# Kernel tuning notes

Hardware: AMD Instinct MI355X
Metric: run time of the kernel (lower is better)

Reference implementation:

```python
import jax, jax.numpy as jnp
import numpy as np

V, BLOCK, L, H, C = 50257, 1024, 4, 12, 768
HS = C // H  # 64
EPS = 1e-6  # flax LayerNorm default


def _ln(x, scale, bias):
    mu = jnp.mean(x, axis=-1, keepdims=True)
    var = jnp.var(x, axis=-1, keepdims=True)
    return (x - mu) * jax.lax.rsqrt(var + EPS) * scale + bias


def setup_inputs() -> dict:
    key = jax.random.key(0)
    ks = jax.random.split(key, 12)
    B, T = 2, 1024
    inp = {
        'idx': jax.random.randint(ks[0], (B, T), 0, V),
        'targets': jax.random.randint(ks[1], (B, T), 0, V),
        'wte': jax.random.normal(ks[2], (V, C), jnp.float32) * 0.02,
        'wpe': jax.random.normal(ks[3], (BLOCK, C), jnp.float32) * 0.02,
        'ln1_s': jnp.ones((L, C), jnp.float32),
        'ln1_b': jnp.zeros((L, C), jnp.float32),
        'attn_k': jax.random.normal(ks[4], (L, C, H, 3 * HS), jnp.float32) * 0.02,
        'attn_b': jnp.zeros((L, H, 3 * HS), jnp.float32),
        'aproj_k': jax.random.normal(ks[5], (L, C, C), jnp.float32) * 0.02,
        'aproj_b': jnp.zeros((L, C), jnp.float32),
        'ln2_s': jnp.ones((L, C), jnp.float32),
        'ln2_b': jnp.zeros((L, C), jnp.float32),
        'fc_k': jax.random.normal(ks[6], (L, C, 4 * C), jnp.float32) * 0.02,
        'fc_b': jnp.zeros((L, 4 * C), jnp.float32),
        'mproj_k': jax.random.normal(ks[7], (L, 4 * C, C), jnp.float32) * 0.02,
        'mproj_b': jnp.zeros((L, C), jnp.float32),
        'lnf_s': jnp.ones((C,), jnp.float32),
        'lnf_b': jnp.zeros((C,), jnp.float32),
    }
    return inp


def _block(x, ln1_s, ln1_b, Wqkv, bqkv, Wo, bo, ln2_s, ln2_b, Wfc, bfc, Wmp, bmp, mask):
    B, T, _ = x.shape
    h = _ln(x, ln1_s, ln1_b)
    qkv = jnp.einsum('btc,chd->bhtd', h, Wqkv) + bqkv[:, None, :]  # [B,H,T,3HS]
    q, k, v = jnp.split(qkv, 3, axis=-1)
    att = jnp.einsum('bhtd,bhsd->bhts', q, k) * (1.0 / jnp.sqrt(jnp.float32(HS)))
    att = jnp.where(mask, att, -jnp.inf)
    att = jax.nn.softmax(att, axis=-1)
    y = jnp.einsum('bhts,bhsd->bthd', att, v).reshape(B, T, C)
    x = x + y @ Wo + bo
    h = _ln(x, ln2_s, ln2_b)
    h = jax.nn.gelu(h @ Wfc + bfc, approximate=True)
    x = x + h @ Wmp + bmp
    return x


def reference(idx, targets, wte, wpe, ln1_s, ln1_b, attn_k, attn_b, aproj_k, aproj_b,
              ln2_s, ln2_b, fc_k, fc_b, mproj_k, mproj_b, lnf_s, lnf_b):
    B, T = idx.shape
    x = wte[idx] + wpe[jnp.arange(T)][None]  # [B,T,C]
    mask = jnp.tril(jnp.ones((T, T), bool))[None, None]
    for l in range(L):
        x = _block(x, ln1_s[l], ln1_b[l], attn_k[l], attn_b[l], aproj_k[l], aproj_b[l],
                   ln2_s[l], ln2_b[l], fc_k[l], fc_b[l], mproj_k[l], mproj_b[l], mask)
    x = _ln(x, lnf_s, lnf_b)
    logits = jnp.einsum('btc,vc->btv', x, wte)  # tied output projection (wte.attend)
    logp = jax.nn.log_softmax(logits, axis=-1)
    loss = -jnp.mean(jnp.take_along_axis(logp, targets[..., None], axis=-1))
    return logits, loss
```

## Files before the change

### kernel.cpp

```cpp
#include <hip/hip_runtime.h>
#include <hip/hip_bf16.h>
#include <math.h>

typedef __attribute__((ext_vector_type(8))) short bf16x8;
typedef __attribute__((ext_vector_type(4))) float f32x4;

static constexpr int Bv   = 2;
static constexpr int Tv   = 1024;
static constexpr int Cv   = 768;
static constexpr int Hv   = 12;
static constexpr int Lv   = 4;
static constexpr int Vv   = 50257;
static constexpr int Mv   = 2048;
static constexpr int NTv  = 393;
static constexpr float EPSv = 1e-6f;

__device__ __forceinline__ void gload16(const void* g, void* l) {
    __builtin_amdgcn_global_load_lds((const __attribute__((address_space(1))) void*)g,
                                     (__attribute__((address_space(3))) void*)l, 16, 0, 0);
}
__device__ __forceinline__ void waitvm0_barrier() {
    asm volatile("s_waitcnt vmcnt(0)" ::: "memory");
    __builtin_amdgcn_s_barrier();
}

__global__ void embed_kernel(const int* __restrict__ idx,
                             const float* __restrict__ wte,
                             const float* __restrict__ wpe,
                             float* __restrict__ x) {
    int row = blockIdx.x;
    int t   = row & (Tv - 1);
    int tok = idx[row];
    const float* src = wte + (size_t)tok * Cv;
    const float* pos = wpe + (size_t)t * Cv;
    float* dst = x + (size_t)row * Cv;
    for (int c = threadIdx.x; c < Cv; c += 256)
        dst[c] = src[c] + pos[c];
}

__device__ __forceinline__ ushort4 pack4bf(float4 v) {
    ushort4 u;
    u.x = __bfloat16_as_ushort(__float2bfloat16(v.x));
    u.y = __bfloat16_as_ushort(__float2bfloat16(v.y));
    u.z = __bfloat16_as_ushort(__float2bfloat16(v.z));
    u.w = __bfloat16_as_ushort(__float2bfloat16(v.w));
    return u;
}

__global__ void ln_kernel(const float* __restrict__ in,
                          const float* __restrict__ sc,
                          const float* __restrict__ bi,
                          __hip_bfloat16* __restrict__ out) {
    int row  = blockIdx.x * 4 + (threadIdx.x >> 6);
    int lane = threadIdx.x & 63;
    const float4* xr = (const float4*)(in + (size_t)row * Cv);
    float4 a = xr[lane], b = xr[lane + 64], c = xr[lane + 128];
    float sum = a.x + a.y + a.z + a.w + b.x + b.y + b.z + b.w + c.x + c.y + c.z + c.w;
    float sq  = a.x*a.x + a.y*a.y + a.z*a.z + a.w*a.w
              + b.x*b.x + b.y*b.y + b.z*b.z + b.w*b.w
              + c.x*c.x + c.y*c.y + c.z*c.z + c.w*c.w;
    #pragma unroll
    for (int off = 32; off; off >>= 1) {
        sum += __shfl_xor(sum, off, 64);
        sq  += __shfl_xor(sq,  off, 64);
    }
    float mean = sum * (1.0f / Cv);
    float var  = sq * (1.0f / Cv) - mean * mean;
    float rs   = rsqrtf(var + EPSv);
    const float4* s4 = (const float4*)sc;
    const float4* b4 = (const float4*)bi;
    ushort4* orow = (ushort4*)(out + (size_t)row * Cv);
    #pragma unroll
    for (int i = 0; i < 3; ++i) {
        float4 v = (i == 0) ? a : (i == 1) ? b : c;
        float4 s = s4[lane + 64 * i];
        float4 t = b4[lane + 64 * i];
        float4 o;
        o.x = (v.x - mean) * rs * s.x + t.x;
        o.y = (v.y - mean) * rs * s.y + t.y;
        o.z = (v.z - mean) * rs * s.z + t.z;
        o.w = (v.w - mean) * rs * s.w + t.w;
        orow[lane + 64 * i] = pack4bf(o);
    }
}

__global__ void wtrans_kernel(const float* __restrict__ in,
                              __hip_bfloat16* __restrict__ out, int K, int N) {
    __shared__ float tile[32][33];
    int k0 = blockIdx.y * 32, n0 = blockIdx.x * 32;
    int tx = threadIdx.x & 31, ty = threadIdx.x >> 5;
    #pragma unroll
    for (int i = 0; i < 4; ++i)
        tile[ty + i * 8][tx] = in[(size_t)(k0 + ty + i * 8) * N + n0 + tx];
    __syncthreads();
    #pragma unroll
    for (int i = 0; i < 4; ++i)
        out[(size_t)(n0 + ty + i * 8) * K + k0 + tx] =
            __float2bfloat16(tile[tx][ty + i * 8]);
}

__global__ void cvt_kernel(const float* __restrict__ in,
                           __hip_bfloat16* __restrict__ out, int n4) {
    int stride = gridDim.x * 256;
    for (int i = blockIdx.x * 256 + threadIdx.x; i < n4; i += stride) {
        float4 v = ((const float4*)in)[i];
        ((ushort4*)out)[i] = pack4bf(v);
    }
}

__global__ void vtrans_kernel(const __hip_bfloat16* __restrict__ qkv,
                              __hip_bfloat16* __restrict__ vt) {
    __shared__ __hip_bfloat16 tile[32][33];
    int bh = blockIdx.z;
    int b = bh / Hv, h = bh % Hv;
    int t0 = blockIdx.x * 32, d0 = blockIdx.y * 32;
    int tx = threadIdx.x & 31, ty = threadIdx.x >> 5;
    #pragma unroll
    for (int i = 0; i < 4; ++i)
        tile[ty + i * 8][tx] =
            qkv[(size_t)(b * Tv + t0 + ty + i * 8) * 2304 + h * 192 + 128 + d0 + tx];
    __syncthreads();
    #pragma unroll
    for (int i = 0; i < 4; ++i)
        vt[((size_t)bh * 64 + d0 + ty + i * 8) * Tv + t0 + tx] = tile[tx][ty + i * 8];
}

template<int EPI, int BM>
__launch_bounds__(256)
__global__ void gemm_bf16(const __hip_bfloat16* __restrict__ A,
                          const __hip_bfloat16* __restrict__ Bt,
                          const float* __restrict__ bias,
                          const float* R, float* Cf,
                          __hip_bfloat16* __restrict__ Cb,
                          int M, int N, int K) {
    constexpr int FM = BM / 32;
    constexpr int NA = BM / 64;
    __shared__ __hip_bfloat16 As[2][BM * 32];
    __shared__ __hip_bfloat16 Bs[2][64 * 32];
    int tid = threadIdx.x;
    int wave = tid >> 6, lane = tid & 63;
    int wr = wave >> 1, wc = wave & 1;
    int rowBase = blockIdx.y * BM, colBase = blockIdx.x * 64;

    f32x4 acc[FM][2] = {};

    int srow  = wave * 16 + (lane >> 2);
    int skcol = (lane & 3) * 8;
    const __hip_bfloat16* Ap0 = A + (size_t)(rowBase + srow) * K + skcol;
    const __hip_bfloat16* Ap1 = (NA > 1) ? (Ap0 + (size_t)64 * K) : Ap0;
    const __hip_bfloat16* Bp0 = Bt + (size_t)(colBase + srow) * K + skcol;
    int ldso = wave * 512;

    int aoff = (wr * (BM / 2) + (lane & 15)) * 32 + (lane >> 4) * 8;
    int boff = (wc * 32 + (lane & 15)) * 32 + (lane >> 4) * 8;

    gload16(Ap0, &As[0][ldso]);
    if constexpr (NA > 1) gload16(Ap1, &As[0][2048 + ldso]);
    gload16(Bp0, &Bs[0][ldso]);
    Ap0 += 32; Ap1 += 32; Bp0 += 32;
    waitvm0_barrier();

    int nt = K / 32;
    for (int t = 0; t < nt - 1; ++t) {
        int cur = t & 1, nxt = cur ^ 1;
        gload16(Ap0, &As[nxt][ldso]);
        if constexpr (NA > 1) gload16(Ap1, &As[nxt][2048 + ldso]);
        gload16(Bp0, &Bs[nxt][ldso]);
        Ap0 += 32; Ap1 += 32; Bp0 += 32;

        bf16x8 av[FM], bv[2];
        #pragma unroll
        for (int m = 0; m < FM; ++m) av[m] = *(const bf16x8*)&As[cur][aoff + m * 512];
        #pragma unroll
        for (int n = 0; n < 2; ++n)  bv[n] = *(const bf16x8*)&Bs[cur][boff + n * 512];
        #pragma unroll
        for (int m = 0; m < FM; ++m)
            #pragma unroll
            for (int n = 0; n < 2; ++n)
                acc[m][n] = __builtin_amdgcn_mfma_f32_16x16x32_bf16(
                    av[m], bv[n], acc[m][n], 0, 0, 0);
        waitvm0_barrier();
    }
    {
        int cur = (nt - 1) & 1;
        bf16x8 av[FM], bv[2];
        #pragma unroll
        for (int m = 0; m < FM; ++m) av[m] = *(const bf16x8*)&As[cur][aoff + m * 512];
        #pragma unroll
        for (int n = 0; n < 2; ++n)  bv[n] = *(const bf16x8*)&Bs[cur][boff + n * 512];
        #pragma unroll
        for (int m = 0; m < FM; ++m)
            #pragma unroll
            for (int n = 0; n < 2; ++n)
                acc[m][n] = __builtin_amdgcn_mfma_f32_16x16x32_bf16(
                    av[m], bv[n], acc[m][n], 0, 0, 0);
    }

    int fq = lane >> 4, fr = lane & 15;
    #pragma unroll
    for (int m = 0; m < FM; ++m) {
        #pragma unroll
        for (int n = 0; n < 2; ++n) {
            f32x4 v = acc[m][n];
            int col = colBase + wc * 32 + n * 16 + fr;
            #pragma unroll
            for (int j = 0; j < 4; ++j) {
                int row = rowBase + wr * (BM / 2) + m * 16 + fq * 4 + j;
                float val = v[j] + bias[col];
                if (EPI == 1) {
                    val += R[(size_t)row * N + col];
                    Cf[(size_t)row * N + col] = val;
                } else {
                    if (EPI == 2) {
                        float u = val;
                        float cc = 0.7978845608028654f * (u + 0.044715f * u * u * u);
                        val = 0.5f * u * (1.0f + tanhf(cc));
                    }
                    Cb[(size_t)row * N + col] = __float2bfloat16(val);
                }
            }
        }
    }
}

__launch_bounds__(256)
__global__ void attn_kernel(const __hip_bfloat16* __restrict__ qkv,
                            const __hip_bfloat16* __restrict__ vt,
                            __hip_bfloat16* __restrict__ att) {
    __shared__ __hip_bfloat16 Qs[64 * 64];
    __shared__ __hip_bfloat16 Ks[64 * 64];
    __shared__ __hip_bfloat16 Vs[64 * 64];
    __shared__ __hip_bfloat16 Ps[64 * 64];
    int bh = blockIdx.x;
    int b = bh / Hv, h = bh % Hv;
    int qt = (int)gridDim.y - 1 - (int)blockIdx.y;
    int q0 = qt * 64;
    int tid = threadIdx.x, wave = tid >> 6, lane = tid & 63;
    int g = lane >> 4, fr = lane & 15;
    int srow8 = lane >> 3, sc8 = lane & 7;

    const __hip_bfloat16* qbase = qkv + (size_t)(b * Tv + q0) * 2304 + h * 192;
    #pragma unroll
    for (int i = 0; i < 2; ++i) {
        int row = wave * 16 + i * 8 + srow8;
        gload16(qbase + (size_t)row * 2304 + ((sc8 ^ (row & 7)) * 8),
                Qs + (wave * 16 + i * 8) * 64);
    }

    f32x4 accO[4] = {};
    float mrun[4] = {-1e30f, -1e30f, -1e30f, -1e30f};
    float lrun[4] = {0.f, 0.f, 0.f, 0.f};

    for (int kv = 0; kv <= qt; ++kv) {
        int s0 = kv * 64;
        __syncthreads();
        const __hip_bfloat16* kbase = qkv + (size_t)(b * Tv + s0) * 2304 + h * 192 + 64;
        const __hip_bfloat16* vbase = vt + (size_t)bh * 64 * Tv + s0;
        #pragma unroll
        for (int i = 0; i < 2; ++i) {
            int row = wave * 16 + i * 8 + srow8;
            gload16(kbase + (size_t)row * 2304 + ((sc8 ^ (row & 7)) * 8),
                    Ks + (wave * 16 + i * 8) * 64);
            gload16(vbase + (size_t)row * Tv + ((sc8 ^ (row & 7)) * 8),
                    Vs + (wave * 16 + i * 8) * 64);
        }
        __syncthreads();

        f32x4 s4[4] = {};
        #pragma unroll
        for (int kk = 0; kk < 2; ++kk) {
            int qrow = wave * 16 + fr;
            bf16x8 qa = *(const bf16x8*)&Qs[qrow * 64 + (((g + 4 * kk) ^ (fr & 7)) * 8)];
            #pragma unroll
            for (int n = 0; n < 4; ++n) {
                int krow = n * 16 + fr;
                bf16x8 kb = *(const bf16x8*)&Ks[krow * 64 + (((g + 4 * kk) ^ (fr & 7)) * 8)];
                s4[n] = __builtin_amdgcn_mfma_f32_16x16x32_bf16(qa, kb, s4[n], 0, 0, 0);
            }
        }

        bool dia = (kv == qt);
        #pragma unroll
        for (int j = 0; j < 4; ++j) {
            int qg = q0 + wave * 16 + g * 4 + j;
            float sj[4], mx = -1e30f;
            #pragma unroll
            for (int n = 0; n < 4; ++n) {
                float v = s4[n][j] * 0.125f;
                if (dia && (s0 + n * 16 + fr) > qg) v = -1e30f;
                sj[n] = v;
                mx = fmaxf(mx, v);
            }
            #pragma unroll
            for (int off = 1; off < 16; off <<= 1)
                mx = fmaxf(mx, __shfl_xor(mx, off, 64));
            float mnew = fmaxf(mrun[j], mx);
            float ps = 0.f;
            unsigned short pb[4];
            #pragma unroll
            for (int n = 0; n < 4; ++n) {
                float p = __expf(sj[n] - mnew);
                __hip_bfloat16 pc = __float2bfloat16(p);
                pb[n] = __bfloat16_as_ushort(pc);
                ps += __bfloat162float(pc);
            }
            #pragma unroll
            for (int off = 1; off < 16; off <<= 1)
                ps += __shfl_xor(ps, off, 64);
            float cr = __expf(mrun[j] - mnew);
            lrun[j] = lrun[j] * cr + ps;
            mrun[j] = mnew;
            int prow = wave * 16 + g * 4 + j;
            #pragma unroll
            for (int n = 0; n < 4; ++n) {
                int byteoff = (32 * n + 2 * fr) ^ ((prow & 7) << 4);
                ((unsigned short*)Ps)[prow * 64 + (byteoff >> 1)] = pb[n];
            }
            #pragma unroll
            for (int n = 0; n < 4; ++n) accO[n][j] *= cr;
        }
        __syncthreads();

        #pragma unroll
        for (int kk = 0; kk < 2; ++kk) {
            int prow = wave * 16 + fr;
            bf16x8 pa = *(const bf16x8*)&Ps[prow * 64 + (((g + 4 * kk) ^ (fr & 7)) * 8)];
            #pragma unroll
            for (int n = 0; n < 4; ++n) {
                int vrow = n * 16 + fr;
                bf16x8 vb = *(const bf16x8*)&Vs[vrow * 64 + (((g + 4 * kk) ^ (fr & 7)) * 8)];
                accO[n] = __builtin_amdgcn_mfma_f32_16x16x32_bf16(pa, vb, accO[n], 0, 0, 0);
            }
        }
    }

    #pragma unroll
    for (int j = 0; j < 4; ++j) {
        float inv = 1.0f / lrun[j];
        int row = b * Tv + q0 + wave * 16 + g * 4 + j;
        #pragma unroll
        for (int n = 0; n < 4; ++n)
            att[(size_t)row * Cv + h * 64 + n * 16 + fr] =
                __float2bfloat16(accO[n][j] * inv);
    }
}

__launch_bounds__(256)
__global__ void lmhead_kernel(const __hip_bfloat16* __restrict__ A,
                              const __hip_bfloat16* __restrict__ Bt,
                              float* __restrict__ Cf,
                              float* __restrict__ pLse) {
    constexpr int K = Cv, N = Vv;
    __shared__ __hip_bfloat16 As[2][4096];
    __shared__ __hip_bfloat16 Bs[2][4096];
    __shared__ float ps2[2][128];

    int bid = blockIdx.x;
    int nid = (bid & 7) * (NTv * 16 / 8) + (bid >> 3);
    int rowT = nid & 15, colT = nid >> 4;
    int rowBase = rowT * 128, colBase = colT * 128;

    int tid = threadIdx.x, wave = tid >> 6, lane = tid & 63;
    int wr = wave >> 1, wc = wave & 1;

    f32x4 acc[4][4] = {};

    int srow  = wave * 16 + (lane >> 2);
    int skcol = (lane & 3) * 8;
    const __hip_bfloat16* Ap  = A + (size_t)(rowBase + srow) * K + skcol;
    const __hip_bfloat16* Ap2 = Ap + (size_t)64 * K;
    int brow1 = colBase + srow;
    int brow2 = brow1 + 64;
    const __hip_bfloat16* Bp  = Bt + (size_t)brow1 * K + skcol;
    const __hip_bfloat16* Bp2 = Bt + (size_t)(brow2 < N ? brow2 : N - 1) * K + skcol;
    int ldso = wave * 512;

    int aoff = (wr * 64 + (lane & 15)) * 32 + (lane >> 4) * 8;
    int boff = (wc * 64 + (lane & 15)) * 32 + (lane >> 4) * 8;

    gload16(Ap,  &As[0][ldso]);
    gload16(Ap2, &As[0][2048 + ldso]);
    gload16(Bp,  &Bs[0][ldso]);
    gload16(Bp2, &Bs[0][2048 + ldso]);
    Ap += 32; Ap2 += 32; Bp += 32; Bp2 += 32;
    waitvm0_barrier();

    constexpr int nt = K / 32;
    for (int t = 0; t < nt - 1; ++t) {
        int cur = t & 1, nxt = cur ^ 1;
        gload16(Ap,  &As[nxt][ldso]);
        gload16(Ap2, &As[nxt][2048 + ldso]);
        gload16(Bp,  &Bs[nxt][ldso]);
        gload16(Bp2, &Bs[nxt][2048 + ldso]);
        Ap += 32; Ap2 += 32; Bp += 32; Bp2 += 32;

        bf16x8 av[4], bv[4];
        #pragma unroll
        for (int m = 0; m < 4; ++m) av[m] = *(const bf16x8*)&As[cur][aoff + m * 512];
        #pragma unroll
        for (int n = 0; n < 4; ++n) bv[n] = *(const bf16x8*)&Bs[cur][boff + n * 512];
        #pragma unroll
        for (int m = 0; m < 4; ++m)
            #pragma unroll
            for (int n = 0; n < 4; ++n)
                acc[m][n] = __builtin_amdgcn_mfma_f32_16x16x32_bf16(
                    av[m], bv[n], acc[m][n], 0, 0, 0);
        waitvm0_barrier();
    }
    {
        int cur = (nt - 1) & 1;
        bf16x8 av[4], bv[4];
        #pragma unroll
        for (int m = 0; m < 4; ++m) av[m] = *(const bf16x8*)&As[cur][aoff + m * 512];
        #pragma unroll
        for (int n = 0; n < 4; ++n) bv[n] = *(const bf16x8*)&Bs[cur][boff + n * 512];
        #pragma unroll
        for (int m = 0; m < 4; ++m)
            #pragma unroll
            for (int n = 0; n < 4; ++n)
                acc[m][n] = __builtin_amdgcn_mfma_f32_16x16x32_bf16(
                    av[m], bv[n], acc[m][n], 0, 0, 0);
    }

    int fq = lane >> 4, fr = lane & 15;

    #pragma unroll
    for (int m = 0; m < 4; ++m) {
        #pragma unroll
        for (int j = 0; j < 4; ++j) {
            int row = rowBase + wr * 64 + m * 16 + fq * 4 + j;
            float s = 0.f;
            #pragma unroll
            for (int n = 0; n < 4; ++n) {
                int col = colBase + wc * 64 + n * 16 + fr;
                float v = acc[m][n][j];
                if (col < N) {
                    Cf[(size_t)row * N + col] = v;
                    s += __expf(v);
                }
            }
            #pragma unroll
            for (int off = 1; off < 16; off <<= 1)
                s += __shfl_xor(s, off, 64);
            if (fr == 0)
                ps2[wc][wr * 64 + m * 16 + fq * 4 + j] = s;
        }
    }
    __syncthreads();
    if (tid < 128)
        pLse[(size_t)(rowBase + tid) * NTv + colT] = ps2[0][tid] + ps2[1][tid];
}

__global__ void plse_reduce_kernel(const float* __restrict__ pLse,
                                   const float* __restrict__ logits,
                                   const int* __restrict__ targets,
                                   float* __restrict__ rloss) {
    int row  = blockIdx.x * 4 + (threadIdx.x >> 6);
    int lane = threadIdx.x & 63;
    const float* pr = pLse + (size_t)row * NTv;
    float l = 0.f;
    for (int i = lane; i < NTv; i += 64) l += pr[i];
    #pragma unroll
    for (int off = 32; off; off >>= 1) l += __shfl_xor(l, off, 64);
    if (lane == 0)
        rloss[row] = logf(l) - logits[(size_t)row * Vv + targets[row]];
}

__global__ void loss_final_kernel(const float* __restrict__ rloss,
                                  float* __restrict__ out, int out_size) {
    float s = 0.f;
    for (int i = threadIdx.x; i < Mv; i += 256) s += rloss[i];
    #pragma unroll
    for (int off = 32; off; off >>= 1) s += __shfl_xor(s, off, 64);
    __shared__ float sw[4];
    int wave = threadIdx.x >> 6, lane = threadIdx.x & 63;
    if (lane == 0) sw[wave] = s;
    __syncthreads();
    if (threadIdx.x == 0)
        out[out_size - 1] = (sw[0] + sw[1] + sw[2] + sw[3]) / (float)Mv;
}

extern "C" void kernel_launch(void* const* d_in, const int* in_sizes, int n_in,
                              void* d_out, int out_size, void* d_ws, size_t ws_size,
                              hipStream_t stream) {
    const int*   idx     = (const int*)  d_in[0];
    const int*   targets = (const int*)  d_in[1];
    const float* wte     = (const float*)d_in[2];
    const float* wpe     = (const float*)d_in[3];
    const float* ln1_s   = (const float*)d_in[4];
    const float* ln1_b   = (const float*)d_in[5];
    const float* attn_k  = (const float*)d_in[6];
    const float* attn_b  = (const float*)d_in[7];
    const float* aproj_k = (const float*)d_in[8];
    const float* aproj_b = (const float*)d_in[9];
    const float* ln2_s   = (const float*)d_in[10];
    const float* ln2_b   = (const float*)d_in[11];
    const float* fc_k    = (const float*)d_in[12];
    const float* fc_b    = (const float*)d_in[13];
    const float* mproj_k = (const float*)d_in[14];
    const float* mproj_b = (const float*)d_in[15];
    const float* lnf_s   = (const float*)d_in[16];
    const float* lnf_b   = (const float*)d_in[17];

    float* out = (float*)d_out;
    char* ws  = (char*)d_ws;
    char* ob  = (char*)d_out;

    constexpr size_t NEED = 83568128ULL;
    if (ws_size < NEED) return;

    __hip_bfloat16* wte_bf = (__hip_bfloat16*)(ws + 0);
    __hip_bfloat16* h_bf   = (__hip_bfloat16*)(ws + 77194752);
    float*          pLse   = (float*)(ws + 80340480);
    float*          rloss  = (float*)(ws + 83559936);

    float*          x      = (float*)(ob + 0);
    __hip_bfloat16* qkv_bf = (__hip_bfloat16*)(ob + 6291456);
    __hip_bfloat16* vt_bf  = (__hip_bfloat16*)(ob + 15728640);
    __hip_bfloat16* att_bf = (__hip_bfloat16*)(ob + 18874368);
    __hip_bfloat16* fco_bf = (__hip_bfloat16*)(ob + 22020096);
    __hip_bfloat16* w0     = (__hip_bfloat16*)(ob + 34603008);
    __hip_bfloat16* w1     = (__hip_bfloat16*)(ob + 38141952);
    __hip_bfloat16* w2     = (__hip_bfloat16*)(ob + 39321600);
    __hip_bfloat16* w3     = (__hip_bfloat16*)(ob + 44040192);

    embed_kernel<<<Mv, 256, 0, stream>>>(idx, wte, wpe, x);

    for (int l = 0; l < Lv; ++l) {
        wtrans_kernel<<<dim3(72, 24), 256, 0, stream>>>(
            attn_k + (size_t)l * Cv * 2304, w0, Cv, 2304);
        wtrans_kernel<<<dim3(24, 24), 256, 0, stream>>>(
            aproj_k + (size_t)l * Cv * Cv, w1, Cv, Cv);
        wtrans_kernel<<<dim3(96, 24), 256, 0, stream>>>(
            fc_k + (size_t)l * Cv * 3072, w2, Cv, 3072);
        wtrans_kernel<<<dim3(24, 96), 256, 0, stream>>>(
            mproj_k + (size_t)l * 3072 * Cv, w3, 3072, Cv);

        ln_kernel<<<512, 256, 0, stream>>>(x, ln1_s + l * Cv, ln1_b + l * Cv, h_bf);
        gemm_bf16<0, 128><<<dim3(36, 16), 256, 0, stream>>>(
            h_bf, w0, attn_b + l * 2304, nullptr, nullptr, qkv_bf, Mv, 2304, Cv);
        vtrans_kernel<<<dim3(32, 2, 24), 256, 0, stream>>>(qkv_bf, vt_bf);
        attn_kernel<<<dim3(24, 16), 256, 0, stream>>>(qkv_bf, vt_bf, att_bf);
        gemm_bf16<1, 64><<<dim3(12, 32), 256, 0, stream>>>(
            att_bf, w1, aproj_b + l * Cv, x, x, nullptr, Mv, Cv, Cv);
        ln_kernel<<<512, 256, 0, stream>>>(x, ln2_s + l * Cv, ln2_b + l * Cv, h_bf);
        gemm_bf16<2, 128><<<dim3(48, 16), 256, 0, stream>>>(
            h_bf, w2, fc_b + l * 3072, nullptr, nullptr, fco_bf, Mv, 3072, Cv);
        gemm_bf16<1, 64><<<dim3(12, 32), 256, 0, stream>>>(
            fco_bf, w3, mproj_b + l * Cv, x, x, nullptr, Mv, Cv, 3072);
    }

    ln_kernel<<<512, 256, 0, stream>>>(x, lnf_s, lnf_b, h_bf);
    cvt_kernel<<<2048, 256, 0, stream>>>(wte, wte_bf, (Vv * Cv) / 4);
    lmhead_kernel<<<16 * NTv, 256, 0, stream>>>(h_bf, wte_bf, out, pLse);
    plse_reduce_kernel<<<512, 256, 0, stream>>>(pLse, out, targets, rloss);
    loss_final_kernel<<<1, 256, 0, stream>>>(rloss, out, out_size);
}
```

Before: 1.063 ms.

## Triple-buffer LDS tiles with partial vmcnt waits in GEMM and LM head

Both the generic bf16 GEMM and the LM-head GEMM move from double buffering to three LDS stages, keeping two tiles of global-to-LDS loads in flight. Partial s_waitcnt vmcnt counts replace full drains, and an lgkmcnt barrier after the fragment reads lets the next stage overwrite the buffer just consumed. The aim is to hide global load latency behind MFMA work. The cost is 50% more LDS per block, which may lower occupancy, especially in the LM head at 48KB.

```diff
diff --git a/kernel.cpp b/kernel.cpp
--- a/kernel.cpp
+++ b/kernel.cpp
@@ -19,9 +19,17 @@
     __builtin_amdgcn_global_load_lds((const __attribute__((address_space(1))) void*)g,
                                      (__attribute__((address_space(3))) void*)l, 16, 0, 0);
 }
-__device__ __forceinline__ void waitvm0_barrier() {
-    asm volatile("s_waitcnt vmcnt(0)" ::: "memory");
-    __builtin_amdgcn_s_barrier();
+template<int N>
+__device__ __forceinline__ void waitvm_barrier() {
+    if constexpr (N == 0)      asm volatile("s_waitcnt vmcnt(0)\ns_barrier" ::: "memory");
+    else if constexpr (N == 2) asm volatile("s_waitcnt vmcnt(2)\ns_barrier" ::: "memory");
+    else if constexpr (N == 3) asm volatile("s_waitcnt vmcnt(3)\ns_barrier" ::: "memory");
+    else if constexpr (N == 4) asm volatile("s_waitcnt vmcnt(4)\ns_barrier" ::: "memory");
+    else if constexpr (N == 6) asm volatile("s_waitcnt vmcnt(6)\ns_barrier" ::: "memory");
+    else                       asm volatile("s_waitcnt vmcnt(8)\ns_barrier" ::: "memory");
+}
+__device__ __forceinline__ void lgkm0_barrier() {
+    asm volatile("s_waitcnt lgkmcnt(0)\ns_barrier" ::: "memory");
 }
 
 __global__ void embed_kernel(const int* __restrict__ idx,
@@ -133,10 +141,11 @@
                           const float* R, float* Cf,
                           __hip_bfloat16* __restrict__ Cb,
                           int M, int N, int K) {
-    constexpr int FM = BM / 32;
-    constexpr int NA = BM / 64;
-    __shared__ __hip_bfloat16 As[2][BM * 32];
-    __shared__ __hip_bfloat16 Bs[2][64 * 32];
+    constexpr int FM  = BM / 32;
+    constexpr int NA  = BM / 64;
+    constexpr int LPT = NA + 1;
+    __shared__ __hip_bfloat16 As[3][BM * 32];
+    __shared__ __hip_bfloat16 Bs[3][64 * 32];
     int tid = threadIdx.x;
     int wave = tid >> 6, lane = tid & 63;
     int wr = wave >> 1, wc = wave & 1;
@@ -154,46 +163,40 @@
     int aoff = (wr * (BM / 2) + (lane & 15)) * 32 + (lane >> 4) * 8;
     int boff = (wc * 32 + (lane & 15)) * 32 + (lane >> 4) * 8;
 
-    gload16(Ap0, &As[0][ldso]);
-    if constexpr (NA > 1) gload16(Ap1, &As[0][2048 + ldso]);
-    gload16(Bp0, &Bs[0][ldso]);
-    Ap0 += 32; Ap1 += 32; Bp0 += 32;
-    waitvm0_barrier();
+    auto stage = [&](int buf) {
+        gload16(Ap0, &As[buf][ldso]);
+        if constexpr (NA > 1) gload16(Ap1, &As[buf][2048 + ldso]);
+        gload16(Bp0, &Bs[buf][ldso]);
+        Ap0 += 32;
+        if constexpr (NA > 1) Ap1 += 32;
+        Bp0 += 32;
+    };
+
+    stage(0); stage(1); stage(2);
 
     int nt = K / 32;
-    for (int t = 0; t < nt - 1; ++t) {
-        int cur = t & 1, nxt = cur ^ 1;
-        gload16(Ap0, &As[nxt][ldso]);
-        if constexpr (NA > 1) gload16(Ap1, &As[nxt][2048 + ldso]);
-        gload16(Bp0, &Bs[nxt][ldso]);
-        Ap0 += 32; Ap1 += 32; Bp0 += 32;
+    int cur = 0;
+    for (int t = 0; t < nt; ++t) {
+        if (t < nt - 2)       waitvm_barrier<2 * LPT>();
+        else if (t == nt - 2) waitvm_barrier<LPT>();
+        else                  waitvm_barrier<0>();
 
         bf16x8 av[FM], bv[2];
         #pragma unroll
         for (int m = 0; m < FM; ++m) av[m] = *(const bf16x8*)&As[cur][aoff + m * 512];
         #pragma unroll
         for (int n = 0; n < 2; ++n)  bv[n] = *(const bf16x8*)&Bs[cur][boff + n * 512];
+        lgkm0_barrier();
+
+        if (t + 3 < nt) stage(cur);
+
         #pragma unroll
         for (int m = 0; m < FM; ++m)
             #pragma unroll
             for (int n = 0; n < 2; ++n)
                 acc[m][n] = __builtin_amdgcn_mfma_f32_16x16x32_bf16(
                     av[m], bv[n], acc[m][n], 0, 0, 0);
-        waitvm0_barrier();
-    }
-    {
-        int cur = (nt - 1) & 1;
-        bf16x8 av[FM], bv[2];
-        #pragma unroll
-        for (int m = 0; m < FM; ++m) av[m] = *(const bf16x8*)&As[cur][aoff + m * 512];
-        #pragma unroll
-        for (int n = 0; n < 2; ++n)  bv[n] = *(const bf16x8*)&Bs[cur][boff + n * 512];
-        #pragma unroll
-        for (int m = 0; m < FM; ++m)
-            #pragma unroll
-            for (int n = 0; n < 2; ++n)
-                acc[m][n] = __builtin_amdgcn_mfma_f32_16x16x32_bf16(
-                    av[m], bv[n], acc[m][n], 0, 0, 0);
+        cur = (cur == 2) ? 0 : cur + 1;
     }
 
     int fq = lane >> 4, fr = lane & 15;
@@ -351,8 +354,8 @@
                               float* __restrict__ Cf,
                               float* __restrict__ pLse) {
     constexpr int K = Cv, N = Vv;
-    __shared__ __hip_bfloat16 As[2][4096];
-    __shared__ __hip_bfloat16 Bs[2][4096];
+    __shared__ __hip_bfloat16 As[3][4096];
+    __shared__ __hip_bfloat16 Bs[3][4096];
     __shared__ float ps2[2][128];
 
     int bid = blockIdx.x;
@@ -378,48 +381,39 @@
     int aoff = (wr * 64 + (lane & 15)) * 32 + (lane >> 4) * 8;
     int boff = (wc * 64 + (lane & 15)) * 32 + (lane >> 4) * 8;
 
-    gload16(Ap,  &As[0][ldso]);
-    gload16(Ap2, &As[0][2048 + ldso]);
-    gload16(Bp,  &Bs[0][ldso]);
-    gload16(Bp2, &Bs[0][2048 + ldso]);
-    Ap += 32; Ap2 += 32; Bp += 32; Bp2 += 32;
-    waitvm0_barrier();
+    auto stage = [&](int buf) {
+        gload16(Ap,  &As[buf][ldso]);
+        gload16(Ap2, &As[buf][2048 + ldso]);
+        gload16(Bp,  &Bs[buf][ldso]);
+        gload16(Bp2, &Bs[buf][2048 + ldso]);
+        Ap += 32; Ap2 += 32; Bp += 32; Bp2 += 32;
+    };
+
+    stage(0); stage(1); stage(2);
 
     constexpr int nt = K / 32;
-    for (int t = 0; t < nt - 1; ++t) {
-        int cur = t & 1, nxt = cur ^ 1;
-        gload16(Ap,  &As[nxt][ldso]);
-        gload16(Ap2, &As[nxt][2048 + ldso]);
-        gload16(Bp,  &Bs[nxt][ldso]);
-        gload16(Bp2, &Bs[nxt][2048 + ldso]);
-        Ap += 32; Ap2 += 32; Bp += 32; Bp2 += 32;
+    int cur = 0;
+    for (int t = 0; t < nt; ++t) {
+        if (t < nt - 2)       waitvm_barrier<8>();
+        else if (t == nt - 2) waitvm_barrier<4>();
+        else                  waitvm_barrier<0>();
 
         bf16x8 av[4], bv[4];
         #pragma unroll
         for (int m = 0; m < 4; ++m) av[m] = *(const bf16x8*)&As[cur][aoff + m * 512];
         #pragma unroll
         for (int n = 0; n < 4; ++n) bv[n] = *(const bf16x8*)&Bs[cur][boff + n * 512];
+        lgkm0_barrier();
+
+        if (t + 3 < nt) stage(cur);
+
         #pragma unroll
         for (int m = 0; m < 4; ++m)
             #pragma unroll
             for (int n = 0; n < 4; ++n)
                 acc[m][n] = __builtin_amdgcn_mfma_f32_16x16x32_bf16(
                     av[m], bv[n], acc[m][n], 0, 0, 0);
-        waitvm0_barrier();
-    }
-    {
-        int cur = (nt - 1) & 1;
-        bf16x8 av[4], bv[4];
-        #pragma unroll
-        for (int m = 0; m < 4; ++m) av[m] = *(const bf16x8*)&As[cur][aoff + m * 512];
-        #pragma unroll
-        for (int n = 0; n < 4; ++n) bv[n] = *(const bf16x8*)&Bs[cur][boff + n * 512];
-        #pragma unroll
-        for (int m = 0; m < 4; ++m)
-            #pragma unroll
-            for (int n = 0; n < 4; ++n)
-                acc[m][n] = __builtin_amdgcn_mfma_f32_16x16x32_bf16(
-                    av[m], bv[n], acc[m][n], 0, 0, 0);
+        cur = (cur == 2) ? 0 : cur + 1;
     }
 
     int fq = lane >> 4, fr = lane & 15;
```

After: 986.8 us. 1.08x faster.
